# Kernel optimization log

Hardware: AMD Instinct MI355X
Metric: run time of the kernel (lower is better)

## Reference

```python
import jax, jax.numpy as jnp
import numpy as np
import math

T = 120      # frame_num == audio_len == max_seq_len
D = 64       # hidden_layer_size
H = 2        # n_head
DH = D // H
DFF = 2 * D
DOUT = 31
PERIOD = 10
EPS = 1e-5
NEG = -1e9
SCALE = 1.0 / math.sqrt(DH)
SLOPES = (1.0 / 16.0, 1.0 / 256.0)  # ALiBi slopes for n_head=2


def _pe():
    # PeriodicPositionalEncoding: sinusoid over one period, tiled
    pos = jnp.arange(PERIOD, dtype=jnp.float32)[:, None]
    div = jnp.exp(jnp.arange(0, D, 2, dtype=jnp.float32) * (-math.log(10000.0) / D))
    s, c = jnp.sin(pos * div), jnp.cos(pos * div)
    pe = jnp.stack([s, c], axis=-1).reshape(PERIOD, D)  # interleave sin/cos
    return jnp.tile(pe, (T // PERIOD + 1, 1))[:T]


def _alibi_mask():
    # causal mask + ALiBi bias: alibi[i,j] = -slope * floor((i-j)/period) for j<=i
    slopes = jnp.array(SLOPES, dtype=jnp.float32)
    i = jnp.arange(T)[:, None]
    j = jnp.arange(T)[None, :]
    rel = ((i - j) // PERIOD).astype(jnp.float32)
    return jnp.where(j <= i, -slopes[:, None, None] * rel, NEG)  # [H,T,T]


def _ln(x, g, b):
    m = x.mean(-1, keepdims=True)
    v = ((x - m) ** 2).mean(-1, keepdims=True)
    return (x - m) / jnp.sqrt(v + EPS) * g + b


def setup_inputs() -> dict:
    key = jax.random.key(0)
    ks = iter(jax.random.split(key, 32))
    n = lambda shape, s=0.05: jax.random.normal(next(ks), shape, dtype=jnp.float32) * s
    inp = {
        'audio': jax.random.normal(next(ks), (1, T, 1024), dtype=jnp.float32),
        'W_audio': n((D, 1024)), 'b_audio': n((D,)),
        'obj_W': n((D, 5)),
        'Wq': n((D, D)), 'bq': n((D,)), 'Wk': n((D, D)), 'bk': n((D,)),
        'Wv': n((D, D)), 'bv': n((D,)), 'Wo': n((D, D)), 'bo': n((D,)),
        'Wv2': n((D, D)), 'bv2': n((D,)), 'Wo2': n((D, D)), 'bo2': n((D,)),
        'g1': jnp.ones((D,)), 'be1': jnp.zeros((D,)),
        'g2': jnp.ones((D,)), 'be2': jnp.zeros((D,)),
        'g3': jnp.ones((D,)), 'be3': jnp.zeros((D,)),
        'W1': n((DFF, D)), 'c1': n((DFF,)), 'W2': n((D, DFF)), 'c2': n((D,)),
        'Wr': n((DOUT, D)), 'br': n((DOUT,)), 'Wm': n((D, DOUT)), 'bm': n((D,)),
    }
    return inp


def _forward(audio, W_audio, b_audio, obj_W, Wq, bq, Wk, bk, Wv, bv, Wo, bo,
             Wv2, bv2, Wo2, bo2, g1, be1, g2, be2, g3, be3,
             W1, c1, W2, c2, Wr, br, Wm, bm):
    mem = audio[0] @ W_audio.T + b_audio          # [S,D], S == T
    style = obj_W[:, 0]                            # obj_vector @ [1,0,0,0,0]
    pe = _pe()
    mask = _alibi_mask()
    slopes = jnp.array(SLOPES, dtype=jnp.float32)
    jarr = jnp.arange(T)

    # enc_dec_mask leaves exactly one memory key per target row (anti-diagonal
    # from the end); the feedback row t at step t always attends memory[-1],
    # so its cross-attn output is just the projected value of the last frame.
    cross_last = (mem[-1] @ Wv2.T + bv2) @ Wo2.T + bo2  # [D]

    def step(emb, t):
        # decode only the last row (row t) of the growing sequence; 1-layer
        # post-norm decoder => row t depends only on input rows 0..t.
        x = emb + pe                                 # PPE over prefix
        xq = jnp.take(x, t, axis=0)                  # [D]
        q = (xq @ Wq.T + bq).reshape(H, DH)
        k = (x @ Wk.T + bk).reshape(T, H, DH)
        v = (x @ Wv.T + bv).reshape(T, H, DH)
        bias = jnp.where(jarr <= t,
                         -slopes[:, None] * ((t - jarr) // PERIOD).astype(jnp.float32),
                         NEG)                        # [H,T]
        sc = jnp.einsum('hd,shd->hs', q, k) * SCALE + bias
        a = jax.nn.softmax(sc, axis=-1)
        sa = jnp.einsum('hs,shd->hd', a, v).reshape(D) @ Wo.T + bo
        h1 = _ln(xq + sa, g1, be1)
        h2 = _ln(h1 + cross_last, g2, be2)
        h3 = _ln(h2 + jax.nn.relu(h2 @ W1.T + c1) @ W2.T + c2, g3, be3)
        new = (h3 @ Wr.T + br) @ Wm.T + bm + style   # vertice_map(vertice_map_r(.)) + style
        emb = jax.lax.dynamic_update_slice(emb, new[None, :], (t + 1, 0))
        return emb, None

    emb0 = jnp.zeros((T, D), audio.dtype).at[0].set(style)
    emb, _ = jax.lax.scan(step, emb0, jnp.arange(T - 1))

    # final full-length decode (last loop iteration of the torch module)
    x = emb + pe
    q = (x @ Wq.T + bq).reshape(T, H, DH)
    k = (x @ Wk.T + bk).reshape(T, H, DH)
    v = (x @ Wv.T + bv).reshape(T, H, DH)
    sc = jnp.einsum('thd,shd->hts', q, k) * SCALE + mask
    a = jax.nn.softmax(sc, axis=-1)
    sa = jnp.einsum('hts,shd->thd', a, v).reshape(T, D) @ Wo.T + bo
    h1 = _ln(x + sa, g1, be1)
    # at length T with S == T the enc_dec_mask aligns target row j <-> memory row j
    cross = (mem @ Wv2.T + bv2) @ Wo2.T + bo2
    h2 = _ln(h1 + cross, g2, be2)
    h3 = _ln(h2 + jax.nn.relu(h2 @ W1.T + c1) @ W2.T + c2, g3, be3)
    return (h3 @ Wr.T + br)[None]                    # [1,T,31]


def reference(audio, W_audio, b_audio, obj_W, Wq, bq, Wk, bk, Wv, bv, Wo, bo,
              Wv2, bv2, Wo2, bo2, g1, be1, g2, be2, g3, be3,
              W1, c1, W2, c2, Wr, br, Wm, bm):
    return _forward(audio, W_audio, b_audio, obj_W, Wq, bq, Wk, bk, Wv, bv, Wo, bo,
                    Wv2, bv2, Wo2, bo2, g1, be1, g2, be2, g3, be3,
                    W1, c1, W2, c2, Wr, br, Wm, bm)
```

## Files before the change

kernel.cpp:

```cpp
#include <hip/hip_runtime.h>

typedef unsigned short u16;
typedef unsigned int   u32;
typedef _Float16 f16;
typedef f16 h2 __attribute__((ext_vector_type(2)));
typedef f16 h4 __attribute__((ext_vector_type(4)));
typedef f16 h8 __attribute__((ext_vector_type(8)));

#define T_    120
#define D_    64
#define DOUT_ 31
#define KROW_ 68
#define VROW_ 132

#if defined(__has_builtin)
#if __has_builtin(__builtin_amdgcn_fdot2)
#define DOT2(a,b,c) __builtin_amdgcn_fdot2((a),(b),(c),false)
#endif
#endif
#ifndef DOT2
#define DOT2(a,b,c) ((float)(a).x*(float)(b).x + ((float)(a).y*(float)(b).y + (c)))
#endif
#define SHV(x,i,j) __builtin_shufflevector((x),(x),(i),(j))

__device__ __forceinline__ h2 pk(float a, float b){
#if defined(__has_builtin) && __has_builtin(__builtin_amdgcn_cvt_pkrtz)
  return __builtin_bit_cast(h2, __builtin_amdgcn_cvt_pkrtz(a, b));
#else
  h2 r; r.x = (f16)a; r.y = (f16)b; return r;
#endif
}
__device__ __forceinline__ float b2f(u16 u){ return __uint_as_float(((u32)u) << 16); }
__device__ __forceinline__ float2 bp2(u32 u){
  float2 r; r.x = __uint_as_float(u << 16); r.y = __uint_as_float(u & 0xffff0000u); return r;
}
__device__ __forceinline__ u16 f2bu(float f){
  u32 u = __float_as_uint(f);
  u32 r = u + 0x7fffu + ((u >> 16) & 1u);
  return (u16)(r >> 16);
}
__device__ __forceinline__ u16 f2h16(float x){
  f16 v = (f16)x; u16 r; __builtin_memcpy(&r, &v, 2); return r;
}
__device__ __forceinline__ float fast_rcp(float x){
#if defined(__has_builtin) && __has_builtin(__builtin_amdgcn_rcpf)
  return __builtin_amdgcn_rcpf(x);
#else
  return 1.f / x;
#endif
}
#define WSYNC() do{ __asm__ __volatile__("" ::: "memory"); __builtin_amdgcn_wave_barrier(); }while(0)

__device__ __forceinline__ float dpp_sum(float x){
  int t;
  t = __builtin_amdgcn_update_dpp(0, __float_as_int(x), 0x111, 0xf, 0xf, true); x += __int_as_float(t);
  t = __builtin_amdgcn_update_dpp(0, __float_as_int(x), 0x112, 0xf, 0xf, true); x += __int_as_float(t);
  t = __builtin_amdgcn_update_dpp(0, __float_as_int(x), 0x114, 0xf, 0xf, true); x += __int_as_float(t);
  t = __builtin_amdgcn_update_dpp(0, __float_as_int(x), 0x118, 0xf, 0xf, true); x += __int_as_float(t);
  t = __builtin_amdgcn_update_dpp(0, __float_as_int(x), 0x142, 0xf, 0xf, true); x += __int_as_float(t);
  t = __builtin_amdgcn_update_dpp(0, __float_as_int(x), 0x143, 0xf, 0xf, true); x += __int_as_float(t);
  return __int_as_float(__builtin_amdgcn_readlane(__float_as_int(x), 63));
}
__device__ __forceinline__ float dpp_max_pos(float x){
  int t;
  t = __builtin_amdgcn_update_dpp(0, __float_as_int(x), 0x111, 0xf, 0xf, true); x = fmaxf(x, __int_as_float(t));
  t = __builtin_amdgcn_update_dpp(0, __float_as_int(x), 0x112, 0xf, 0xf, true); x = fmaxf(x, __int_as_float(t));
  t = __builtin_amdgcn_update_dpp(0, __float_as_int(x), 0x114, 0xf, 0xf, true); x = fmaxf(x, __int_as_float(t));
  t = __builtin_amdgcn_update_dpp(0, __float_as_int(x), 0x118, 0xf, 0xf, true); x = fmaxf(x, __int_as_float(t));
  t = __builtin_amdgcn_update_dpp(0, __float_as_int(x), 0x142, 0xf, 0xf, true); x = fmaxf(x, __int_as_float(t));
  t = __builtin_amdgcn_update_dpp(0, __float_as_int(x), 0x143, 0xf, 0xf, true); x = fmaxf(x, __int_as_float(t));
  return __int_as_float(__builtin_amdgcn_readlane(__float_as_int(x), 63));
}
__device__ __forceinline__ float pe_val(int row, int i){
  const float coef = -0.28782313662425574f;
  int p = row % 10;
  float dv  = __expf((float)(i >> 1) * coef);
  float ang = (float)p * dv;
  return (i & 1) ? __cosf(ang) : __sinf(ang);
}
__device__ __forceinline__ void loadrow32(h2* dst, const float* row){
  #pragma unroll
  for (int r = 0; r < 16; ++r){
    float4 f = ((const float4*)row)[r];
    dst[2*r]   = pk(f.x, f.y);
    dst[2*r+1] = pk(f.z, f.w);
  }
}

__global__ __launch_bounds__(256) void k_pre(const float* __restrict__ audio,
                                             const float* __restrict__ Wa, const float* __restrict__ ba,
                                             const float* __restrict__ Wv2, const float* __restrict__ bv2,
                                             const float* __restrict__ Wo2, const float* __restrict__ bo2,
                                             const float* __restrict__ Wo, const float* __restrict__ W1,
                                             const float* __restrict__ W2, const float* __restrict__ Wr,
                                             const float* __restrict__ Wm, const float* __restrict__ br,
                                             const float* __restrict__ bm,
                                             float* __restrict__ cross, float* __restrict__ Ms,
                                             float* __restrict__ bMv,
                                             u16* __restrict__ wob, u16* __restrict__ w1b,
                                             u16* __restrict__ w2b, u16* __restrict__ wrb){
  const int b = blockIdx.x, tid = threadIdx.x;
  if (b == 120){
    for (int i = tid; i < 4096; i += 256) wob[i] = f2bu(Wo[i]);
    for (int i = tid; i < 8192; i += 256){ w1b[i] = f2bu(W1[i]); w2b[i] = f2bu(W2[i]); }
    for (int i = tid; i < 1984; i += 256) wrb[i] = f2bu(Wr[i]);
    for (int idx = tid; idx < 4096; idx += 256){
      int d = idx >> 6, e = idx & 63;
      float acc = 0.f;
      #pragma unroll
      for (int j = 0; j < 31; ++j) acc += Wm[d*31 + j] * Wr[j*64 + e];
      Ms[idx] = acc;
    }
    if (tid < 64){
      float acc = bm[tid];
      #pragma unroll
      for (int j = 0; j < 31; ++j) acc += Wm[tid*31 + j] * br[j];
      bMv[tid] = acc;
    }
    return;
  }
  __shared__ float ash[1024];
  __shared__ float msh[64], tsh[64];
  for (int i = tid; i < 1024; i += 256) ash[i] = audio[b*1024 + i];
  __syncthreads();
  const int w = tid >> 6, lane = tid & 63;
  for (int d = w*16; d < w*16 + 16; ++d){
    const float4* row = (const float4*)(Wa + d*1024);
    float acc = 0.f;
    #pragma unroll
    for (int m = 0; m < 4; ++m){
      float4 wp = row[lane + 64*m];
      int j = 4*(lane + 64*m);
      acc += wp.x*ash[j] + wp.y*ash[j+1] + wp.z*ash[j+2] + wp.w*ash[j+3];
    }
    acc = dpp_sum(acc);
    if (lane == 0) msh[d] = acc + ba[d];
  }
  __syncthreads();
  if (tid < 64){
    const float4* r1 = (const float4*)(Wv2 + tid*64);
    float a = bv2[tid];
    #pragma unroll
    for (int j = 0; j < 16; ++j){ float4 p = r1[j]; a += p.x*msh[4*j] + p.y*msh[4*j+1] + p.z*msh[4*j+2] + p.w*msh[4*j+3]; }
    tsh[tid] = a;
  }
  __syncthreads();
  if (tid < 64){
    const float4* r2 = (const float4*)(Wo2 + tid*64);
    float c = bo2[tid];
    #pragma unroll
    for (int j = 0; j < 16; ++j){ float4 p = r2[j]; c += p.x*tsh[4*j] + p.y*tsh[4*j+1] + p.z*tsh[4*j+2] + p.w*tsh[4*j+3]; }
    cross[b*64 + tid] = c;
  }
}

__global__ __launch_bounds__(128, 1) void k_scan(
    const float* __restrict__ objW,
    const float* __restrict__ Wq, const float* __restrict__ bq,
    const float* __restrict__ Wk, const float* __restrict__ bk,
    const float* __restrict__ Wv, const float* __restrict__ bv,
    const float* __restrict__ Wo, const float* __restrict__ bo,
    const float* __restrict__ g1, const float* __restrict__ be1,
    const float* __restrict__ g2, const float* __restrict__ be2,
    const float* __restrict__ g3, const float* __restrict__ be3,
    const float* __restrict__ W1, const float* __restrict__ c1,
    const float* __restrict__ W2, const float* __restrict__ c2,
    const float* __restrict__ Ms, const float* __restrict__ bMv,
    const float* __restrict__ cross,
    u16* __restrict__ xw16, u16* __restrict__ Kw16, u16* __restrict__ Vw16)
{
  __shared__ __align__(16) f16 KcS[128*KROW_];
  __shared__ __align__(16) f16 VcS[D_*VROW_];
  __shared__ __align__(16) f16 xwS[T_*D_];
  __shared__ __align__(16) f16 sch[256];
  __shared__ __align__(16) f16 xh[64], qh[64], h2h[64], h3h[64];
  __shared__ __align__(16) f16 at0h[64], at1h[64];
  __shared__ __align__(16) u32 fsh2[64];
  __shared__ float sa0lo[64], sa0hi[64];
  __shared__ float invSh;
  __shared__ float pe_tab[640];

  const int tid = threadIdx.x;
  const int i = tid & 63;
  const int hh = tid >> 6;
  const bool w0 = tid < 64;

  h2 A[32], B[32], C[32], D[32], E[32], G[64];
  float biasA=0.f, biasB=0.f, bo_r=0.f, c1lo=0.f, c1hi=0.f, c2_r=0.f, cls_r=0.f;
  float g1r=0.f,b1r=0.f,g2r=0.f,b2r=0.f;
  float mg_r=0.f, u_r=0.f;
  float x_r = 0.f;

  {
    const int qi = hh*32 + (i & 31);
    if (i < 32){ loadrow32(A, Wq + qi*64); biasA = bq[qi]; }
    else       { loadrow32(A, Wk + qi*64); biasA = bk[qi]; }
    loadrow32(C, Wo + i*64);
  }
  if (w0){
    loadrow32(B, Wv + i*64);
    biasB = bv[i];
  } else {
    loadrow32(B, W1 + i*64);
    loadrow32(D, W1 + (64+i)*64);
    {
      const float4* lo4 = (const float4*)(W2 + i*128);
      const float4* hi4 = (const float4*)(W2 + i*128 + 64);
      #pragma unroll
      for (int r = 0; r < 16; ++r){
        float4 a = lo4[r], b = hi4[r];
        G[4*r+0] = pk(a.x, b.x);
        G[4*r+1] = pk(a.y, b.y);
        G[4*r+2] = pk(a.z, b.z);
        G[4*r+3] = pk(a.w, b.w);
      }
    }
    {
      const float4* mr  = (const float4*)(Ms + i*64);
      const float4* gv  = (const float4*)g3;
      const float4* b3v = (const float4*)be3;
      float mg = 0.f, mb = 0.f;
      #pragma unroll
      for (int r = 0; r < 16; ++r){
        float4 f = mr[r], g = gv[r], b = b3v[r];
        float e0 = f.x*g.x, e1 = f.y*g.y, e2 = f.z*g.z, e3 = f.w*g.w;
        E[2*r]   = pk(e0, e1);
        E[2*r+1] = pk(e2, e3);
        mg += (e0+e1)+(e2+e3);
        mb += f.x*b.x + f.y*b.y + f.z*b.z + f.w*b.w;
      }
      mg_r = mg;
      u_r  = bMv[i] + objW[i*5] + mb;
    }
    bo_r = bo[i]; c1lo = c1[i]; c1hi = c1[64+i]; c2_r = c2[i];
    g1r = g1[i]; b1r = be1[i]; g2r = g2[i]; b2r = be2[i];
    cls_r = cross[119*64 + i];
  }
  { u32* p = (u32*)KcS; for (int idx = tid; idx < 128*KROW_/2; idx += 128) p[idx] = 0; }
  { u32* p = (u32*)VcS; for (int idx = tid; idx < D_*VROW_/2;  idx += 128) p[idx] = 0; }
  for (int idx = tid; idx < 640; idx += 128) pe_tab[idx] = pe_val(idx >> 6, idx & 63);
  if (!w0){
    float x0 = objW[i*5] + pe_val(0, i);
    x_r = x0; xh[i] = (f16)x0; xwS[i] = (f16)x0;
  }
  __syncthreads();

  int pp = 1;
  for (int t = 0; t < T_-1; ++t){
    float e0r, e1r, inv_w, lo_w = 0.f, hi_w = 0.f;
    h8 xr[8];
    {
      const h8* xv = (const h8*)xh;
      #pragma unroll
      for (int r = 0; r < 8; ++r) xr[r] = xv[r];
      float a0=biasA,a1=0.f,a2=0.f,a3=0.f;
      #pragma unroll
      for (int r = 0; r < 8; ++r){
        h8 x = xr[r];
        a0 = DOT2(A[4*r+0], SHV(x,0,1), a0);
        a1 = DOT2(A[4*r+1], SHV(x,2,3), a1);
        a2 = DOT2(A[4*r+2], SHV(x,4,5), a2);
        a3 = DOT2(A[4*r+3], SHV(x,6,7), a3);
      }
      float qk = (a0+a1)+(a2+a3);
      f16* dst = (i < 32) ? (qh + hh*32 + i) : (KcS + t*KROW_ + hh*32 + (i - 32));
      *dst = (f16)qk;
    }
    WSYNC();
    {
      if (w0){
        float v0=biasB,v1=0.f,v2=0.f,v3=0.f;
        #pragma unroll
        for (int r = 0; r < 8; ++r){
          h8 x = xr[r];
          v0 = DOT2(B[4*r+0], SHV(x,0,1), v0); v1 = DOT2(B[4*r+1], SHV(x,2,3), v1);
          v2 = DOT2(B[4*r+2], SHV(x,4,5), v2); v3 = DOT2(B[4*r+3], SHV(x,6,7), v3);
        }
        VcS[i*VROW_ + t] = (f16)((v0+v1)+(v2+v3));
      }
      const int j = i;
      const h8* qv = (const h8*)(qh + hh*32);
      const h4* k0 = (const h4*)(KcS + j*KROW_ + hh*32);
      const h4* k1 = (const h4*)(KcS + (j+64)*KROW_ + hh*32);
      float d0a=0.f,d0b=0.f,d1a=0.f,d1b=0.f;
      #pragma unroll
      for (int r = 0; r < 4; ++r){
        h8 q = qv[r];
        h4 ka = k0[2*r], kb = k0[2*r+1], kc = k1[2*r], kd = k1[2*r+1];
        d0a = DOT2(SHV(ka,0,1), SHV(q,0,1), d0a);
        d0b = DOT2(SHV(ka,2,3), SHV(q,2,3), d0b);
        d0a = DOT2(SHV(kb,0,1), SHV(q,4,5), d0a);
        d0b = DOT2(SHV(kb,2,3), SHV(q,6,7), d0b);
        d1a = DOT2(SHV(kc,0,1), SHV(q,0,1), d1a);
        d1b = DOT2(SHV(kc,2,3), SHV(q,2,3), d1b);
        d1a = DOT2(SHV(kd,0,1), SHV(q,4,5), d1a);
        d1b = DOT2(SHV(kd,2,3), SHV(q,6,7), d1b);
      }
      float d0 = d0a + d0b, d1 = d1a + d1b;
      const float slope = hh ? 0.00390625f : 0.0625f;
      int r0 = (t - j) / 10, r1 = (t - j - 64) / 10;
      float s0 = d0*0.17677669529663687f - slope*(float)r0;
      float s1 = d1*0.17677669529663687f - slope*(float)r1;
      e0r = (j      <= t) ? __expf(fminf(s0, 8.f)) : 0.f;
      e1r = (j + 64 <= t) ? __expf(fminf(s1, 8.f)) : 0.f;
      sch[hh*128 + j]      = (f16)e0r;
      sch[hh*128 + j + 64] = (f16)e1r;
    }
    __syncthreads();
    {
      float den = dpp_sum(e0r + e1r);
      inv_w = fast_rcp(den);
      if (tid == 0) invSh = inv_w;
      if (w0 || t >= 64){
        const int hd = i >> 5;
        const h8* av = (const h8*)(sch + hd*128) + (w0 ? 0 : 8);
        const h4* vv = (const h4*)(VcS + i*VROW_) + (w0 ? 0 : 16);
        float p0=0.f,p1=0.f,p2=0.f,p3=0.f;
        #pragma unroll
        for (int r = 0; r < 8; ++r){
          h8 a = av[r];
          h4 va = vv[2*r], vb = vv[2*r+1];
          p0 = DOT2(SHV(va,0,1), SHV(a,0,1), p0);
          p1 = DOT2(SHV(va,2,3), SHV(a,2,3), p1);
          p2 = DOT2(SHV(vb,0,1), SHV(a,4,5), p2);
          p3 = DOT2(SHV(vb,2,3), SHV(a,6,7), p3);
        }
        float p = (p0+p1)+(p2+p3);
        f16* ath = w0 ? at0h : at1h;
        ath[i] = (f16)p;
        WSYNC();
        const h8* pv = (const h8*)ath;
        float l0=0.f,l1=0.f,q0=0.f,q1=0.f;
        #pragma unroll
        for (int r = 0; r < 4; ++r){
          h8 x = pv[r];
          l0 = DOT2(C[4*r+0], SHV(x,0,1), l0); l1 = DOT2(C[4*r+1], SHV(x,2,3), l1);
          l0 = DOT2(C[4*r+2], SHV(x,4,5), l0); l1 = DOT2(C[4*r+3], SHV(x,6,7), l1);
        }
        #pragma unroll
        for (int r = 4; r < 8; ++r){
          h8 x = pv[r];
          q0 = DOT2(C[4*r+0], SHV(x,0,1), q0); q1 = DOT2(C[4*r+1], SHV(x,2,3), q1);
          q0 = DOT2(C[4*r+2], SHV(x,4,5), q0); q1 = DOT2(C[4*r+3], SHV(x,6,7), q1);
        }
        lo_w = l0 + l1;  hi_w = q0 + q1;
      }
      if (w0){ sa0lo[i] = lo_w; sa0hi[i] = hi_w; }
    }
    __syncthreads();
    if (!w0){
      float lo0 = sa0lo[i], hi0 = sa0hi[i];
      float inv0 = invSh;
      float pe_c = pe_tab[pp*64 + i];
      float sa = bo_r + inv0*(lo0 + lo_w) + inv_w*(hi0 + hi_w);
      float y = x_r + sa;
      float s = dpp_sum(y), s2 = dpp_sum(y*y);
      float m = s*(1.f/64.f), var = fmaxf(s2*(1.f/64.f) - m*m, 0.f);
      float h1 = (y - m)*rsqrtf(var + 1e-5f)*g1r + b1r;
      float z = h1 + cls_r;
      float sz = dpp_sum(z), sz2 = dpp_sum(z*z);
      float mz = sz*(1.f/64.f), vz = fmaxf(sz2*(1.f/64.f) - mz*mz, 0.f);
      float h2v = (z - mz)*rsqrtf(vz + 1e-5f)*g2r + b2r;
      h2h[i] = (f16)h2v;
      WSYNC();
      h8 hr[8];
      {
        const h8* hv = (const h8*)h2h;
        #pragma unroll
        for (int r = 0; r < 8; ++r) hr[r] = hv[r];
      }
      float a0=c1lo, a1=0.f, a2=0.f, a3=0.f;
      float b0=c1hi, b1=0.f, b2=0.f, b3=0.f;
      #pragma unroll
      for (int r = 0; r < 8; ++r){
        h8 x = hr[r];
        a0 = DOT2(B[4*r+0], SHV(x,0,1), a0);
        a1 = DOT2(B[4*r+1], SHV(x,2,3), a1);
        a2 = DOT2(B[4*r+2], SHV(x,4,5), a2);
        a3 = DOT2(B[4*r+3], SHV(x,6,7), a3);
        b0 = DOT2(D[4*r+0], SHV(x,0,1), b0);
        b1 = DOT2(D[4*r+1], SHV(x,2,3), b1);
        b2 = DOT2(D[4*r+2], SHV(x,4,5), b2);
        b3 = DOT2(D[4*r+3], SHV(x,6,7), b3);
      }
      float fLo = fmaxf((a0+a1)+(a2+a3), 0.f);
      float fHi = fmaxf((b0+b1)+(b2+b3), 0.f);
      fsh2[i] = __builtin_bit_cast(u32, pk(fLo, fHi));
      WSYNC();
      const h8* fv = (const h8*)fsh2;
      float f0=c2_r, f1=0.f, f2=0.f, f3=0.f;
      #pragma unroll
      for (int r = 0; r < 16; ++r){
        h8 x = fv[r];
        f0 = DOT2(G[4*r+0], SHV(x,0,1), f0);
        f1 = DOT2(G[4*r+1], SHV(x,2,3), f1);
        f2 = DOT2(G[4*r+2], SHV(x,4,5), f2);
        f3 = DOT2(G[4*r+3], SHV(x,6,7), f3);
      }
      float y3 = h2v + (f0+f1)+(f2+f3);
      h3h[i] = (f16)y3;
      WSYNC();
      const h8* yv3 = (const h8*)h3h;
      h8 yr[8];
      #pragma unroll
      for (int r = 0; r < 8; ++r) yr[r] = yv3[r];
      float s3 = dpp_sum(y3), s32 = dpp_sum(y3*y3);
      float m3 = s3*(1.f/64.f), v3 = fmaxf(s32*(1.f/64.f) - m3*m3, 0.f);
      float invs = rsqrtf(v3 + 1e-5f);
      float m0=0.f, m1=0.f, m2=0.f, mm3=0.f;
      #pragma unroll
      for (int r = 0; r < 8; ++r){
        h8 x = yr[r];
        m0 = DOT2(E[4*r+0], SHV(x,0,1), m0);
        m1 = DOT2(E[4*r+1], SHV(x,2,3), m1);
        m2 = DOT2(E[4*r+2], SHV(x,4,5), m2);
        mm3 = DOT2(E[4*r+3], SHV(x,6,7), mm3);
      }
      float xn = ((m0+m1)+(m2+mm3))*invs + (u_r - m3*invs*mg_r) + pe_c;
      x_r = xn;
      xh[i] = (f16)xn;
      xwS[(t+1)*64 + i] = (f16)xn;
    }
    __syncthreads();
    pp = (pp == 9) ? 0 : pp + 1;
  }
  {
    const h8* xv = (const h8*)xh;
    h8 xr[8];
    #pragma unroll
    for (int r = 0; r < 8; ++r) xr[r] = xv[r];
    if (w0){
      float v0=biasB,v1=0.f,v2=0.f,v3=0.f;
      #pragma unroll
      for (int r = 0; r < 8; ++r){
        h8 x = xr[r];
        v0 = DOT2(B[4*r+0], SHV(x,0,1), v0);
        v1 = DOT2(B[4*r+1], SHV(x,2,3), v1);
        v2 = DOT2(B[4*r+2], SHV(x,4,5), v2);
        v3 = DOT2(B[4*r+3], SHV(x,6,7), v3);
      }
      Vw16[119*64 + i] = f2h16((v0+v1)+(v2+v3));
    }
    if (i >= 32){
      float k0=biasA,k1=0.f,k2=0.f,k3=0.f;
      #pragma unroll
      for (int r = 0; r < 8; ++r){
        h8 x = xr[r];
        k0 = DOT2(A[4*r+0], SHV(x,0,1), k0);
        k1 = DOT2(A[4*r+1], SHV(x,2,3), k1);
        k2 = DOT2(A[4*r+2], SHV(x,4,5), k2);
        k3 = DOT2(A[4*r+3], SHV(x,6,7), k3);
      }
      Kw16[119*64 + hh*32 + (i-32)] = f2h16((k0+k1)+(k2+k3));
    }
  }
  {
    const u16* kc = (const u16*)KcS;
    const u16* vc = (const u16*)VcS;
    for (int idx = tid; idx < 119*64; idx += 128){
      int t_ = idx >> 6, d = idx & 63;
      Kw16[idx] = kc[t_*KROW_ + d];
      Vw16[idx] = vc[d*VROW_ + t_];
    }
    const u32* xs32 = (const u32*)xwS;
    for (int idx = tid; idx < T_*D_/2; idx += 128) ((u32*)xw16)[idx] = xs32[idx];
  }
}

__global__ __launch_bounds__(128) void k_final(
    const float* __restrict__ Wq, const float* __restrict__ bq, const float* __restrict__ bo,
    const float* __restrict__ g1, const float* __restrict__ be1,
    const float* __restrict__ g2, const float* __restrict__ be2,
    const float* __restrict__ g3, const float* __restrict__ be3,
    const float* __restrict__ c1, const float* __restrict__ c2, const float* __restrict__ br,
    const u16* __restrict__ wo_b, const u16* __restrict__ w1_b,
    const u16* __restrict__ w2_b, const u16* __restrict__ wr_b,
    const float* __restrict__ cross, const u16* __restrict__ xw16,
    const u16* __restrict__ Kw16, const u16* __restrict__ Vw16,
    float* __restrict__ out)
{
  __shared__ float xs[64], qs[64], at[64], h2s[64], h3s[64], fs[128], sc[256];
  const int irow = blockIdx.x, tid = threadIdx.x;
  const f16* xp = (const f16*)xw16;
  const f16* kp = (const f16*)Kw16;
  const f16* vp = (const f16*)Vw16;
  if (tid < 64) xs[tid] = (float)xp[irow*64 + tid];
  __syncthreads();
  if (tid < 64){
    const float4* wr_ = (const float4*)(Wq + tid*64);
    float acc = bq[tid];
    #pragma unroll
    for (int j = 0; j < 16; ++j){ float4 w = wr_[j]; acc += w.x*xs[4*j] + w.y*xs[4*j+1] + w.z*xs[4*j+2] + w.w*xs[4*j+3]; }
    qs[tid] = acc;
  }
  __syncthreads();
  {
    const int h = tid >> 6, j = tid & 63;
    const float* qh_ = qs + h*32;
    float d0 = 0.f, d1 = 0.f;
    const h4* k0 = (const h4*)(kp + j*64 + h*32);
    #pragma unroll
    for (int w = 0; w < 8; ++w){
      h4 p = k0[w];
      d0 += (float)p.x*qh_[4*w] + (float)p.y*qh_[4*w+1] + (float)p.z*qh_[4*w+2] + (float)p.w*qh_[4*w+3];
    }
    if (j < 56){
      const h4* k1 = (const h4*)(kp + (j+64)*64 + h*32);
      #pragma unroll
      for (int w = 0; w < 8; ++w){
        h4 p = k1[w];
        d1 += (float)p.x*qh_[4*w] + (float)p.y*qh_[4*w+1] + (float)p.z*qh_[4*w+2] + (float)p.w*qh_[4*w+3];
      }
    }
    const float slope = h ? 0.00390625f : 0.0625f;
    float s0 = (j      <= irow) ? d0*0.17677669529663687f - slope*(float)((irow-j)/10)    : -1e30f;
    float s1 = (j + 64 <= irow) ? d1*0.17677669529663687f - slope*(float)((irow-j-64)/10) : -1e30f;
    float m = dpp_max_pos(fmaxf(s0, s1) + 16384.f) - 16384.f;
    float e0 = (j      <= irow) ? __expf(s0 - m) : 0.f;
    float e1 = (j + 64 <= irow) ? __expf(s1 - m) : 0.f;
    float inv = 1.f / dpp_sum(e0 + e1);
    sc[h*128 + j]      = e0*inv;
    sc[h*128 + j + 64] = e1*inv;
  }
  __syncthreads();
  if (tid < 64){
    const float* a = sc + (tid >> 5)*128;
    float a0=0.f,a1=0.f,a2=0.f,a3=0.f;
    #pragma unroll
    for (int jj = 0; jj < 30; ++jj){
      a0 += a[4*jj]   * (float)vp[(4*jj)*64   + tid];
      a1 += a[4*jj+1] * (float)vp[(4*jj+1)*64 + tid];
      a2 += a[4*jj+2] * (float)vp[(4*jj+2)*64 + tid];
      a3 += a[4*jj+3] * (float)vp[(4*jj+3)*64 + tid];
    }
    at[tid] = (a0+a1)+(a2+a3);
  }
  __syncthreads();
  if (tid < 64){
    const u32* orow = (const u32*)(wo_b + tid*64);
    float acc = bo[tid];
    #pragma unroll
    for (int w = 0; w < 32; ++w){ float2 p = bp2(orow[w]); acc += p.x*at[2*w] + p.y*at[2*w+1]; }
    float y = xs[tid] + acc;
    float s = dpp_sum(y), s2 = dpp_sum(y*y);
    float m = s*(1.f/64.f), var = fmaxf(s2*(1.f/64.f) - m*m, 0.f);
    float h1 = (y - m)*rsqrtf(var + 1e-5f)*g1[tid] + be1[tid];
    float z = h1 + cross[irow*64 + tid];
    float sz = dpp_sum(z), sz2 = dpp_sum(z*z);
    float mz = sz*(1.f/64.f), vz = fmaxf(sz2*(1.f/64.f) - mz*mz, 0.f);
    h2s[tid] = (z - mz)*rsqrtf(vz + 1e-5f)*g2[tid] + be2[tid];
  }
  __syncthreads();
  {
    const u32* w1r = (const u32*)(w1_b + tid*64);
    float acc = c1[tid];
    #pragma unroll
    for (int w = 0; w < 32; ++w){ float2 p = bp2(w1r[w]); acc += p.x*h2s[2*w] + p.y*h2s[2*w+1]; }
    fs[tid] = fmaxf(acc, 0.f);
  }
  __syncthreads();
  if (tid < 64){
    const u32* w2r = (const u32*)(w2_b + tid*128);
    float acc = c2[tid];
    #pragma unroll
    for (int w = 0; w < 64; ++w){ float2 p = bp2(w2r[w]); acc += p.x*fs[2*w] + p.y*fs[2*w+1]; }
    float y = h2s[tid] + acc;
    float s = dpp_sum(y), s2 = dpp_sum(y*y);
    float m = s*(1.f/64.f), var = fmaxf(s2*(1.f/64.f) - m*m, 0.f);
    h3s[tid] = (y - m)*rsqrtf(var + 1e-5f)*g3[tid] + be3[tid];
  }
  __syncthreads();
  if (tid < DOUT_){
    const u32* rr = (const u32*)(wr_b + tid*64);
    float acc = br[tid];
    #pragma unroll
    for (int w = 0; w < 32; ++w){ float2 p = bp2(rr[w]); acc += p.x*h3s[2*w] + p.y*h3s[2*w+1]; }
    out[irow*DOUT_ + tid] = acc;
  }
}

extern "C" void kernel_launch(void* const* d_in, const int* in_sizes, int n_in,
                              void* d_out, int out_size, void* d_ws, size_t ws_size,
                              hipStream_t stream){
  const float* audio=(const float*)d_in[0];
  const float* Wa   =(const float*)d_in[1];
  const float* ba   =(const float*)d_in[2];
  const float* objW =(const float*)d_in[3];
  const float* Wq   =(const float*)d_in[4];
  const float* bq   =(const float*)d_in[5];
  const float* Wk   =(const float*)d_in[6];
  const float* bk   =(const float*)d_in[7];
  const float* Wv   =(const float*)d_in[8];
  const float* bv   =(const float*)d_in[9];
  const float* Wo   =(const float*)d_in[10];
  const float* bo   =(const float*)d_in[11];
  const float* Wv2  =(const float*)d_in[12];
  const float* bv2  =(const float*)d_in[13];
  const float* Wo2  =(const float*)d_in[14];
  const float* bo2  =(const float*)d_in[15];
  const float* g1   =(const float*)d_in[16];
  const float* be1  =(const float*)d_in[17];
  const float* g2   =(const float*)d_in[18];
  const float* be2  =(const float*)d_in[19];
  const float* g3   =(const float*)d_in[20];
  const float* be3  =(const float*)d_in[21];
  const float* W1   =(const float*)d_in[22];
  const float* c1   =(const float*)d_in[23];
  const float* W2   =(const float*)d_in[24];
  const float* c2   =(const float*)d_in[25];
  const float* Wr   =(const float*)d_in[26];
  const float* br   =(const float*)d_in[27];
  const float* Wm   =(const float*)d_in[28];
  const float* bm   =(const float*)d_in[29];

  float* ws    = (float*)d_ws;
  float* cross = ws;
  float* Ms    = ws + 7680;
  float* bMv   = ws + 11776;
  u16* xw16 = (u16*)(ws + 11840);
  u16* Kw16 = xw16 + 7680;
  u16* Vw16 = Kw16 + 7680;
  u16* wo_b = Vw16 + 7680;
  u16* w1_b = wo_b + 4096;
  u16* w2_b = w1_b + 8192;
  u16* wr_b = w2_b + 8192;
  float* out = (float*)d_out;

  k_pre  <<<dim3(121), dim3(256), 0, stream>>>(audio, Wa, ba, Wv2, bv2, Wo2, bo2,
                                               Wo, W1, W2, Wr, Wm, br, bm,
                                               cross, Ms, bMv, wo_b, w1_b, w2_b, wr_b);
  k_scan <<<dim3(1),   dim3(128), 0, stream>>>(objW, Wq, bq, Wk, bk, Wv, bv, Wo, bo,
                                               g1, be1, g2, be2, g3, be3,
                                               W1, c1, W2, c2, Ms, bMv,
                                               cross, xw16, Kw16, Vw16);
  k_final<<<dim3(120), dim3(128), 0, stream>>>(Wq, bq, bo, g1, be1, g2, be2, g3, be3,
                                               c1, c2, br, wo_b, w1_b, w2_b, wr_b,
                                               cross, xw16, Kw16, Vw16, out);
}
```

Measured before the change: 390.7 us.

## Split FFN first layer across both waves and move LN1/LN2 to wave 0

Moves the residual and LayerNorm 1/2 stage from wave 1 to wave 0, then splits the FFN first-layer rows between the two waves (wave 0 computes the low 64 hidden units, wave 1 the high 64). Wave 1 then runs the second FFN layer with a 2x64 register layout instead of a packed 64-entry G array. This halves the per-wave serial FFN1 work and cuts wave 1's register footprint, at the cost of two extra block-wide barriers per decode step and round-trips through shared memory for x and h2.

```diff
diff --git a/kernel.cpp b/kernel.cpp
--- a/kernel.cpp
+++ b/kernel.cpp
@@ -175,8 +175,9 @@
   __shared__ __align__(16) f16 sch[256];
   __shared__ __align__(16) f16 xh[64], qh[64], h2h[64], h3h[64];
   __shared__ __align__(16) f16 at0h[64], at1h[64];
-  __shared__ __align__(16) u32 fsh2[64];
-  __shared__ float sa0lo[64], sa0hi[64];
+  __shared__ __align__(16) f16 fsh[128];
+  __shared__ float sa1lo[64], sa1hi[64];
+  __shared__ float h2f[64], xf[64];
   __shared__ float invSh;
   __shared__ float pe_tab[640];
 
@@ -185,11 +186,10 @@
   const int hh = tid >> 6;
   const bool w0 = tid < 64;
 
-  h2 A[32], B[32], C[32], D[32], E[32], G[64];
-  float biasA=0.f, biasB=0.f, bo_r=0.f, c1lo=0.f, c1hi=0.f, c2_r=0.f, cls_r=0.f;
+  h2 A[32], B[32], C[32], D[32], E[32], F[32];
+  float biasA=0.f, biasB=0.f, bo_r=0.f, c1r=0.f, c2_r=0.f, cls_r=0.f;
   float g1r=0.f,b1r=0.f,g2r=0.f,b2r=0.f;
   float mg_r=0.f, u_r=0.f;
-  float x_r = 0.f;
 
   {
     const int qi = hh*32 + (i & 31);
@@ -199,22 +199,15 @@
   }
   if (w0){
     loadrow32(B, Wv + i*64);
-    biasB = bv[i];
+    loadrow32(D, W1 + i*64);
+    biasB = bv[i]; c1r = c1[i];
+    bo_r = bo[i];
+    g1r = g1[i]; b1r = be1[i]; g2r = g2[i]; b2r = be2[i];
+    cls_r = cross[119*64 + i];
   } else {
-    loadrow32(B, W1 + i*64);
-    loadrow32(D, W1 + (64+i)*64);
-    {
-      const float4* lo4 = (const float4*)(W2 + i*128);
-      const float4* hi4 = (const float4*)(W2 + i*128 + 64);
-      #pragma unroll
-      for (int r = 0; r < 16; ++r){
-        float4 a = lo4[r], b = hi4[r];
-        G[4*r+0] = pk(a.x, b.x);
-        G[4*r+1] = pk(a.y, b.y);
-        G[4*r+2] = pk(a.z, b.z);
-        G[4*r+3] = pk(a.w, b.w);
-      }
-    }
+    loadrow32(B, W1 + (64+i)*64);
+    loadrow32(D, W2 + i*128);
+    loadrow32(F, W2 + i*128 + 64);
     {
       const float4* mr  = (const float4*)(Ms + i*64);
       const float4* gv  = (const float4*)g3;
@@ -232,16 +225,14 @@
       mg_r = mg;
       u_r  = bMv[i] + objW[i*5] + mb;
     }
-    bo_r = bo[i]; c1lo = c1[i]; c1hi = c1[64+i]; c2_r = c2[i];
-    g1r = g1[i]; b1r = be1[i]; g2r = g2[i]; b2r = be2[i];
-    cls_r = cross[119*64 + i];
+    c1r = c1[64+i]; c2_r = c2[i];
   }
   { u32* p = (u32*)KcS; for (int idx = tid; idx < 128*KROW_/2; idx += 128) p[idx] = 0; }
   { u32* p = (u32*)VcS; for (int idx = tid; idx < D_*VROW_/2;  idx += 128) p[idx] = 0; }
   for (int idx = tid; idx < 640; idx += 128) pe_tab[idx] = pe_val(idx >> 6, idx & 63);
   if (!w0){
     float x0 = objW[i*5] + pe_val(0, i);
-    x_r = x0; xh[i] = (f16)x0; xwS[i] = (f16)x0;
+    xf[i] = x0; xh[i] = (f16)x0; xwS[i] = (f16)x0;
   }
   __syncthreads();
 
@@ -310,7 +301,7 @@
     {
       float den = dpp_sum(e0r + e1r);
       inv_w = fast_rcp(den);
-      if (tid == 0) invSh = inv_w;
+      if (tid == 64) invSh = inv_w;
       if (w0 || t >= 64){
         const int hd = i >> 5;
         const h8* av = (const h8*)(sch + hd*128) + (w0 ? 0 : 8);
@@ -345,15 +336,16 @@
         }
         lo_w = l0 + l1;  hi_w = q0 + q1;
       }
-      if (w0){ sa0lo[i] = lo_w; sa0hi[i] = hi_w; }
+      if (!w0){ sa1lo[i] = lo_w; sa1hi[i] = hi_w; }
     }
     __syncthreads();
-    if (!w0){
-      float lo0 = sa0lo[i], hi0 = sa0hi[i];
-      float inv0 = invSh;
-      float pe_c = pe_tab[pp*64 + i];
-      float sa = bo_r + inv0*(lo0 + lo_w) + inv_w*(hi0 + hi_w);
-      float y = x_r + sa;
+    if (w0){
+      float xfv = xf[i];
+      float inv1 = invSh;
+      float lo1 = 0.f, hi1 = 0.f;
+      if (t >= 64){ lo1 = sa1lo[i]; hi1 = sa1hi[i]; }
+      float sa = bo_r + inv_w*(lo_w + lo1) + inv1*(hi_w + hi1);
+      float y = xfv + sa;
       float s = dpp_sum(y), s2 = dpp_sum(y*y);
       float m = s*(1.f/64.f), var = fmaxf(s2*(1.f/64.f) - m*m, 0.f);
       float h1 = (y - m)*rsqrtf(var + 1e-5f)*g1r + b1r;
@@ -362,42 +354,56 @@
       float mz = sz*(1.f/64.f), vz = fmaxf(sz2*(1.f/64.f) - mz*mz, 0.f);
       float h2v = (z - mz)*rsqrtf(vz + 1e-5f)*g2r + b2r;
       h2h[i] = (f16)h2v;
-      WSYNC();
-      h8 hr[8];
-      {
-        const h8* hv = (const h8*)h2h;
+      h2f[i] = h2v;
+    }
+    __syncthreads();
+    {
+      const h8* hv = (const h8*)h2h;
+      float a0=c1r, a1=0.f, a2=0.f, a3=0.f;
+      if (w0){
         #pragma unroll
-        for (int r = 0; r < 8; ++r) hr[r] = hv[r];
-      }
-      float a0=c1lo, a1=0.f, a2=0.f, a3=0.f;
-      float b0=c1hi, b1=0.f, b2=0.f, b3=0.f;
+        for (int r = 0; r < 8; ++r){
+          h8 x = hv[r];
+          a0 = DOT2(D[4*r+0], SHV(x,0,1), a0);
+          a1 = DOT2(D[4*r+1], SHV(x,2,3), a1);
+          a2 = DOT2(D[4*r+2], SHV(x,4,5), a2);
+          a3 = DOT2(D[4*r+3], SHV(x,6,7), a3);
+        }
+      } else {
+        #pragma unroll
+        for (int r = 0; r < 8; ++r){
+          h8 x = hv[r];
+          a0 = DOT2(B[4*r+0], SHV(x,0,1), a0);
+          a1 = DOT2(B[4*r+1], SHV(x,2,3), a1);
+          a2 = DOT2(B[4*r+2], SHV(x,4,5), a2);
+          a3 = DOT2(B[4*r+3], SHV(x,6,7), a3);
+        }
+      }
+      fsh[tid] = (f16)fmaxf((a0+a1)+(a2+a3), 0.f);
+    }
+    __syncthreads();
+    if (!w0){
+      float pe_c  = pe_tab[pp*64 + i];
+      float h2v_s = h2f[i];
+      const h8* fv = (const h8*)fsh;
+      float a0=c2_r, a1=0.f, a2=0.f, a3=0.f;
       #pragma unroll
       for (int r = 0; r < 8; ++r){
-        h8 x = hr[r];
-        a0 = DOT2(B[4*r+0], SHV(x,0,1), a0);
-        a1 = DOT2(B[4*r+1], SHV(x,2,3), a1);
-        a2 = DOT2(B[4*r+2], SHV(x,4,5), a2);
-        a3 = DOT2(B[4*r+3], SHV(x,6,7), a3);
-        b0 = DOT2(D[4*r+0], SHV(x,0,1), b0);
-        b1 = DOT2(D[4*r+1], SHV(x,2,3), b1);
-        b2 = DOT2(D[4*r+2], SHV(x,4,5), b2);
-        b3 = DOT2(D[4*r+3], SHV(x,6,7), b3);
-      }
-      float fLo = fmaxf((a0+a1)+(a2+a3), 0.f);
-      float fHi = fmaxf((b0+b1)+(b2+b3), 0.f);
-      fsh2[i] = __builtin_bit_cast(u32, pk(fLo, fHi));
-      WSYNC();
-      const h8* fv = (const h8*)fsh2;
-      float f0=c2_r, f1=0.f, f2=0.f, f3=0.f;
-      #pragma unroll
-      for (int r = 0; r < 16; ++r){
         h8 x = fv[r];
-        f0 = DOT2(G[4*r+0], SHV(x,0,1), f0);
-        f1 = DOT2(G[4*r+1], SHV(x,2,3), f1);
-        f2 = DOT2(G[4*r+2], SHV(x,4,5), f2);
-        f3 = DOT2(G[4*r+3], SHV(x,6,7), f3);
-      }
-      float y3 = h2v + (f0+f1)+(f2+f3);
+        a0 = DOT2(D[4*r+0], SHV(x,0,1), a0);
+        a1 = DOT2(D[4*r+1], SHV(x,2,3), a1);
+        a2 = DOT2(D[4*r+2], SHV(x,4,5), a2);
+        a3 = DOT2(D[4*r+3], SHV(x,6,7), a3);
+      }
+      #pragma unroll
+      for (int r = 0; r < 8; ++r){
+        h8 x = fv[8+r];
+        a0 = DOT2(F[4*r+0], SHV(x,0,1), a0);
+        a1 = DOT2(F[4*r+1], SHV(x,2,3), a1);
+        a2 = DOT2(F[4*r+2], SHV(x,4,5), a2);
+        a3 = DOT2(F[4*r+3], SHV(x,6,7), a3);
+      }
+      float y3 = h2v_s + (a0+a1)+(a2+a3);
       h3h[i] = (f16)y3;
       WSYNC();
       const h8* yv3 = (const h8*)h3h;
@@ -417,7 +423,7 @@
         mm3 = DOT2(E[4*r+3], SHV(x,6,7), mm3);
       }
       float xn = ((m0+m1)+(m2+mm3))*invs + (u_r - m3*invs*mg_r) + pe_c;
-      x_r = xn;
+      xf[i] = xn;
       xh[i] = (f16)xn;
       xwS[(t+1)*64 + i] = (f16)xn;
     }
```

Result: slower. 402.4 us (+3.0%).

## Split recurrent decoder work symmetrically across both wavefronts per head

Applied to the files above, without the earlier changes.

Reassigns work in the sequential decode loop so both 64-lane wavefronts do symmetric halves: V projection, attention-times-V and Wo are split per head, and the FFN hidden layer and W2 are split by half with partial sums exchanged through shared memory. Before, wave 1 alone ran the layer norms and the full FFN while wave 0 idled. The aim is to shorten the serial critical path of each step and cut per-thread register weights. In exchange it adds an extra block barrier for the FFN partial-sum exchange, both waves now run the layer norms redundantly, and the old step-end block barrier becomes a wave-level sync.

```diff
diff --git a/kernel.cpp b/kernel.cpp
--- a/kernel.cpp
+++ b/kernel.cpp
@@ -81,6 +81,14 @@
 __device__ __forceinline__ void loadrow32(h2* dst, const float* row){
   #pragma unroll
   for (int r = 0; r < 16; ++r){
+    float4 f = ((const float4*)row)[r];
+    dst[2*r]   = pk(f.x, f.y);
+    dst[2*r+1] = pk(f.z, f.w);
+  }
+}
+__device__ __forceinline__ void loadrow16(h2* dst, const float* row){
+  #pragma unroll
+  for (int r = 0; r < 8; ++r){
     float4 f = ((const float4*)row)[r];
     dst[2*r]   = pk(f.x, f.y);
     dst[2*r+1] = pk(f.z, f.w);
@@ -174,47 +182,31 @@
   __shared__ __align__(16) f16 xwS[T_*D_];
   __shared__ __align__(16) f16 sch[256];
   __shared__ __align__(16) f16 xh[64], qh[64], h2h[64], h3h[64];
-  __shared__ __align__(16) f16 at0h[64], at1h[64];
-  __shared__ __align__(16) u32 fsh2[64];
-  __shared__ float sa0lo[64], sa0hi[64];
-  __shared__ float invSh;
+  __shared__ __align__(16) f16 at0h[32], at1h[32];
+  __shared__ __align__(16) f16 fsh[128];
+  __shared__ float saP0[64], saP1[64];
+  __shared__ float pP0[64], pP1[64];
   __shared__ float pe_tab[640];
 
   const int tid = threadIdx.x;
   const int i = tid & 63;
   const int hh = tid >> 6;
-  const bool w0 = tid < 64;
-
-  h2 A[32], B[32], C[32], D[32], E[32], G[64];
-  float biasA=0.f, biasB=0.f, bo_r=0.f, c1lo=0.f, c1hi=0.f, c2_r=0.f, cls_r=0.f;
+  const bool w1w = hh != 0;
+
+  h2 A[32], B[32], C[16], D[32], G[32], E[32];
+  float biasA=0.f, biasB=0.f, bo_r=0.f, c1r=0.f, c2_r=0.f, cls_r=0.f;
   float g1r=0.f,b1r=0.f,g2r=0.f,b2r=0.f;
   float mg_r=0.f, u_r=0.f;
-  float x_r = 0.f;
+  float x_r;
 
   {
     const int qi = hh*32 + (i & 31);
     if (i < 32){ loadrow32(A, Wq + qi*64); biasA = bq[qi]; }
     else       { loadrow32(A, Wk + qi*64); biasA = bk[qi]; }
-    loadrow32(C, Wo + i*64);
-  }
-  if (w0){
-    loadrow32(B, Wv + i*64);
-    biasB = bv[i];
-  } else {
-    loadrow32(B, W1 + i*64);
-    loadrow32(D, W1 + (64+i)*64);
-    {
-      const float4* lo4 = (const float4*)(W2 + i*128);
-      const float4* hi4 = (const float4*)(W2 + i*128 + 64);
-      #pragma unroll
-      for (int r = 0; r < 16; ++r){
-        float4 a = lo4[r], b = hi4[r];
-        G[4*r+0] = pk(a.x, b.x);
-        G[4*r+1] = pk(a.y, b.y);
-        G[4*r+2] = pk(a.z, b.z);
-        G[4*r+3] = pk(a.w, b.w);
-      }
-    }
+    loadrow32(B, Wv + qi*64);  biasB = bv[qi];
+    loadrow16(C, Wo + i*64 + hh*32);
+    loadrow32(D, W1 + (hh*64 + i)*64);
+    loadrow32(G, W2 + i*128 + hh*64);
     {
       const float4* mr  = (const float4*)(Ms + i*64);
       const float4* gv  = (const float4*)g3;
@@ -232,22 +224,25 @@
       mg_r = mg;
       u_r  = bMv[i] + objW[i*5] + mb;
     }
-    bo_r = bo[i]; c1lo = c1[i]; c1hi = c1[64+i]; c2_r = c2[i];
+    c1r = c1[hh*64 + i]; c2_r = c2[i]; bo_r = bo[i];
     g1r = g1[i]; b1r = be1[i]; g2r = g2[i]; b2r = be2[i];
     cls_r = cross[119*64 + i];
   }
   { u32* p = (u32*)KcS; for (int idx = tid; idx < 128*KROW_/2; idx += 128) p[idx] = 0; }
   { u32* p = (u32*)VcS; for (int idx = tid; idx < D_*VROW_/2;  idx += 128) p[idx] = 0; }
   for (int idx = tid; idx < 640; idx += 128) pe_tab[idx] = pe_val(idx >> 6, idx & 63);
-  if (!w0){
+  {
     float x0 = objW[i*5] + pe_val(0, i);
-    x_r = x0; xh[i] = (f16)x0; xwS[i] = (f16)x0;
+    x_r = x0;
+    xh[i] = (f16)x0;
+    if (w1w) xwS[i] = (f16)x0;
   }
   __syncthreads();
 
   int pp = 1;
+  const float slope = hh ? 0.00390625f : 0.0625f;
   for (int t = 0; t < T_-1; ++t){
-    float e0r, e1r, inv_w, lo_w = 0.f, hi_w = 0.f;
+    float e0r, e1r;
     h8 xr[8];
     {
       const h8* xv = (const h8*)xh;
@@ -268,7 +263,7 @@
     }
     WSYNC();
     {
-      if (w0){
+      if (i < 32){
         float v0=biasB,v1=0.f,v2=0.f,v3=0.f;
         #pragma unroll
         for (int r = 0; r < 8; ++r){
@@ -276,7 +271,7 @@
           v0 = DOT2(B[4*r+0], SHV(x,0,1), v0); v1 = DOT2(B[4*r+1], SHV(x,2,3), v1);
           v2 = DOT2(B[4*r+2], SHV(x,4,5), v2); v3 = DOT2(B[4*r+3], SHV(x,6,7), v3);
         }
-        VcS[i*VROW_ + t] = (f16)((v0+v1)+(v2+v3));
+        VcS[(hh*32 + i)*VROW_ + t] = (f16)((v0+v1)+(v2+v3));
       }
       const int j = i;
       const h8* qv = (const h8*)(qh + hh*32);
@@ -297,7 +292,6 @@
         d1b = DOT2(SHV(kd,2,3), SHV(q,6,7), d1b);
       }
       float d0 = d0a + d0b, d1 = d1a + d1b;
-      const float slope = hh ? 0.00390625f : 0.0625f;
       int r0 = (t - j) / 10, r1 = (t - j - 64) / 10;
       float s0 = d0*0.17677669529663687f - slope*(float)r0;
       float s1 = d1*0.17677669529663687f - slope*(float)r1;
@@ -306,53 +300,47 @@
       sch[hh*128 + j]      = (f16)e0r;
       sch[hh*128 + j + 64] = (f16)e1r;
     }
-    __syncthreads();
+    WSYNC();
     {
       float den = dpp_sum(e0r + e1r);
-      inv_w = fast_rcp(den);
-      if (tid == 0) invSh = inv_w;
-      if (w0 || t >= 64){
-        const int hd = i >> 5;
-        const h8* av = (const h8*)(sch + hd*128) + (w0 ? 0 : 8);
-        const h4* vv = (const h4*)(VcS + i*VROW_) + (w0 ? 0 : 16);
-        float p0=0.f,p1=0.f,p2=0.f,p3=0.f;
-        #pragma unroll
-        for (int r = 0; r < 8; ++r){
-          h8 a = av[r];
-          h4 va = vv[2*r], vb = vv[2*r+1];
-          p0 = DOT2(SHV(va,0,1), SHV(a,0,1), p0);
-          p1 = DOT2(SHV(va,2,3), SHV(a,2,3), p1);
-          p2 = DOT2(SHV(vb,0,1), SHV(a,4,5), p2);
-          p3 = DOT2(SHV(vb,2,3), SHV(a,6,7), p3);
-        }
-        float p = (p0+p1)+(p2+p3);
-        f16* ath = w0 ? at0h : at1h;
-        ath[i] = (f16)p;
-        WSYNC();
-        const h8* pv = (const h8*)ath;
-        float l0=0.f,l1=0.f,q0=0.f,q1=0.f;
-        #pragma unroll
-        for (int r = 0; r < 4; ++r){
-          h8 x = pv[r];
-          l0 = DOT2(C[4*r+0], SHV(x,0,1), l0); l1 = DOT2(C[4*r+1], SHV(x,2,3), l1);
-          l0 = DOT2(C[4*r+2], SHV(x,4,5), l0); l1 = DOT2(C[4*r+3], SHV(x,6,7), l1);
-        }
-        #pragma unroll
-        for (int r = 4; r < 8; ++r){
-          h8 x = pv[r];
-          q0 = DOT2(C[4*r+0], SHV(x,0,1), q0); q1 = DOT2(C[4*r+1], SHV(x,2,3), q1);
-          q0 = DOT2(C[4*r+2], SHV(x,4,5), q0); q1 = DOT2(C[4*r+3], SHV(x,6,7), q1);
-        }
-        lo_w = l0 + l1;  hi_w = q0 + q1;
-      }
-      if (w0){ sa0lo[i] = lo_w; sa0hi[i] = hi_w; }
+      float inv_w = fast_rcp(den);
+      const int l5 = i & 31;
+      const int d  = hh*32 + l5;
+      const int co = (i & 32) ? 64 : 0;
+      const h8* av = (const h8*)(sch + hh*128 + co);
+      const h4* vv = (const h4*)(VcS + d*VROW_ + co);
+      float p0=0.f,p1=0.f,p2=0.f,p3=0.f;
+      #pragma unroll
+      for (int r = 0; r < 8; ++r){
+        h8 a = av[r];
+        h4 va = vv[2*r], vb = vv[2*r+1];
+        p0 = DOT2(SHV(va,0,1), SHV(a,0,1), p0);
+        p1 = DOT2(SHV(va,2,3), SHV(a,2,3), p1);
+        p2 = DOT2(SHV(vb,0,1), SHV(a,4,5), p2);
+        p3 = DOT2(SHV(vb,2,3), SHV(a,6,7), p3);
+      }
+      float p = (p0+p1)+(p2+p3);
+      p += __shfl_xor(p, 32, 64);
+      f16* ath = hh ? at1h : at0h;
+      ath[l5] = (f16)p;
+      WSYNC();
+      const h8* pv = (const h8*)ath;
+      float w0a=0.f,w1a=0.f,w2a=0.f,w3a=0.f;
+      #pragma unroll
+      for (int r = 0; r < 4; ++r){
+        h8 x = pv[r];
+        w0a = DOT2(C[4*r+0], SHV(x,0,1), w0a);
+        w1a = DOT2(C[4*r+1], SHV(x,2,3), w1a);
+        w2a = DOT2(C[4*r+2], SHV(x,4,5), w2a);
+        w3a = DOT2(C[4*r+3], SHV(x,6,7), w3a);
+      }
+      float* saP = hh ? saP1 : saP0;
+      saP[i] = inv_w * ((w0a+w1a)+(w2a+w3a));
     }
     __syncthreads();
-    if (!w0){
-      float lo0 = sa0lo[i], hi0 = sa0hi[i];
-      float inv0 = invSh;
-      float pe_c = pe_tab[pp*64 + i];
-      float sa = bo_r + inv0*(lo0 + lo_w) + inv_w*(hi0 + hi_w);
+    float h2v;
+    {
+      float sa = bo_r + saP0[i] + saP1[i];
       float y = x_r + sa;
       float s = dpp_sum(y), s2 = dpp_sum(y*y);
       float m = s*(1.f/64.f), var = fmaxf(s2*(1.f/64.f) - m*m, 0.f);
@@ -360,44 +348,37 @@
       float z = h1 + cls_r;
       float sz = dpp_sum(z), sz2 = dpp_sum(z*z);
       float mz = sz*(1.f/64.f), vz = fmaxf(sz2*(1.f/64.f) - mz*mz, 0.f);
-      float h2v = (z - mz)*rsqrtf(vz + 1e-5f)*g2r + b2r;
+      h2v = (z - mz)*rsqrtf(vz + 1e-5f)*g2r + b2r;
       h2h[i] = (f16)h2v;
       WSYNC();
-      h8 hr[8];
-      {
-        const h8* hv = (const h8*)h2h;
-        #pragma unroll
-        for (int r = 0; r < 8; ++r) hr[r] = hv[r];
-      }
-      float a0=c1lo, a1=0.f, a2=0.f, a3=0.f;
-      float b0=c1hi, b1=0.f, b2=0.f, b3=0.f;
+      const h8* hv = (const h8*)h2h;
+      float a0=c1r, a1=0.f, a2=0.f, a3=0.f;
       #pragma unroll
       for (int r = 0; r < 8; ++r){
-        h8 x = hr[r];
-        a0 = DOT2(B[4*r+0], SHV(x,0,1), a0);
-        a1 = DOT2(B[4*r+1], SHV(x,2,3), a1);
-        a2 = DOT2(B[4*r+2], SHV(x,4,5), a2);
-        a3 = DOT2(B[4*r+3], SHV(x,6,7), a3);
-        b0 = DOT2(D[4*r+0], SHV(x,0,1), b0);
-        b1 = DOT2(D[4*r+1], SHV(x,2,3), b1);
-        b2 = DOT2(D[4*r+2], SHV(x,4,5), b2);
-        b3 = DOT2(D[4*r+3], SHV(x,6,7), b3);
-      }
-      float fLo = fmaxf((a0+a1)+(a2+a3), 0.f);
-      float fHi = fmaxf((b0+b1)+(b2+b3), 0.f);
-      fsh2[i] = __builtin_bit_cast(u32, pk(fLo, fHi));
+        h8 x = hv[r];
+        a0 = DOT2(D[4*r+0], SHV(x,0,1), a0);
+        a1 = DOT2(D[4*r+1], SHV(x,2,3), a1);
+        a2 = DOT2(D[4*r+2], SHV(x,4,5), a2);
+        a3 = DOT2(D[4*r+3], SHV(x,6,7), a3);
+      }
+      fsh[hh*64 + i] = (f16)fmaxf((a0+a1)+(a2+a3), 0.f);
       WSYNC();
-      const h8* fv = (const h8*)fsh2;
-      float f0=c2_r, f1=0.f, f2=0.f, f3=0.f;
-      #pragma unroll
-      for (int r = 0; r < 16; ++r){
+      const h8* fv = (const h8*)(fsh + hh*64);
+      float f0=0.f, f1=0.f, f2=0.f, f3=0.f;
+      #pragma unroll
+      for (int r = 0; r < 8; ++r){
         h8 x = fv[r];
         f0 = DOT2(G[4*r+0], SHV(x,0,1), f0);
         f1 = DOT2(G[4*r+1], SHV(x,2,3), f1);
         f2 = DOT2(G[4*r+2], SHV(x,4,5), f2);
         f3 = DOT2(G[4*r+3], SHV(x,6,7), f3);
       }
-      float y3 = h2v + (f0+f1)+(f2+f3);
+      float* pP = hh ? pP1 : pP0;
+      pP[i] = (f0+f1)+(f2+f3);
+    }
+    __syncthreads();
+    {
+      float y3 = h2v + c2_r + pP0[i] + pP1[i];
       h3h[i] = (f16)y3;
       WSYNC();
       const h8* yv3 = (const h8*)h3h;
@@ -416,12 +397,12 @@
         m2 = DOT2(E[4*r+2], SHV(x,4,5), m2);
         mm3 = DOT2(E[4*r+3], SHV(x,6,7), mm3);
       }
-      float xn = ((m0+m1)+(m2+mm3))*invs + (u_r - m3*invs*mg_r) + pe_c;
+      float xn = ((m0+m1)+(m2+mm3))*invs + (u_r - m3*invs*mg_r) + pe_tab[pp*64 + i];
       x_r = xn;
       xh[i] = (f16)xn;
-      xwS[(t+1)*64 + i] = (f16)xn;
-    }
-    __syncthreads();
+      if (w1w) xwS[(t+1)*64 + i] = (f16)xn;
+    }
+    WSYNC();
     pp = (pp == 9) ? 0 : pp + 1;
   }
   {
@@ -429,7 +410,7 @@
     h8 xr[8];
     #pragma unroll
     for (int r = 0; r < 8; ++r) xr[r] = xv[r];
-    if (w0){
+    if (i < 32){
       float v0=biasB,v1=0.f,v2=0.f,v3=0.f;
       #pragma unroll
       for (int r = 0; r < 8; ++r){
@@ -439,9 +420,8 @@
         v2 = DOT2(B[4*r+2], SHV(x,4,5), v2);
         v3 = DOT2(B[4*r+3], SHV(x,6,7), v3);
       }
-      Vw16[119*64 + i] = f2h16((v0+v1)+(v2+v3));
-    }
-    if (i >= 32){
+      Vw16[119*64 + hh*32 + i] = f2h16((v0+v1)+(v2+v3));
+    } else {
       float k0=biasA,k1=0.f,k2=0.f,k3=0.f;
       #pragma unroll
       for (int r = 0; r < 8; ++r){
@@ -454,6 +434,7 @@
       Kw16[119*64 + hh*32 + (i-32)] = f2h16((k0+k1)+(k2+k3));
     }
   }
+  __syncthreads();
   {
     const u16* kc = (const u16*)KcS;
     const u16* vc = (const u16*)VcS;
```

Measured after the change: 354.3 us. -9.3%, faster.
